# Performance work log

Hardware: AMD Instinct MI355X
Metric: run time of the kernel (lower is better)

## Reference

```python
import jax, jax.numpy as jnp
import numpy as np


def soft_threshold24(w):
    """2:4 soft-threshold along the last dim: in each contiguous group of 4,
    zero the two smallest magnitudes and shrink the two largest by the
    second-smallest magnitude (sign(w) * relu(|w| - t))."""
    M, N = w.shape
    g = w.reshape(M, N // 4, 4)
    a = jnp.abs(g)
    thr = jnp.sort(a, axis=-1)[..., 1:2]  # 2nd-smallest magnitude per group
    s = jnp.sign(g) * jnp.maximum(a - thr, 0.0)
    return s.reshape(M, N)


def mm_fp16(a, b):
    """fake_fp8_mm: cast operands to fp16, accumulate in fp32."""
    return jnp.matmul(a.astype(jnp.float16), b.astype(jnp.float16),
                      preferred_element_type=jnp.float32)


def setup_inputs() -> dict:
    key = jax.random.key(0)
    k0, k1, k2, k3 = jax.random.split(key, 4)
    B, S, D, R = 4, 2048, 2048, 512
    return {
        "x": jax.random.normal(k0, (B, S, D), jnp.float32),
        "weight_in": jax.random.normal(k1, (D, R), jnp.float32) * 0.02,
        "weight_out": jax.random.normal(k2, (D, R), jnp.float32) * 0.02,
        "bias": jax.random.normal(k3, (D,), jnp.float32) * 0.01,
        "sparse_scale_in": jnp.array(1.0, jnp.float32),
        "sparse_scale_out": jnp.array(1.0, jnp.float32),
    }


def reference(x, weight_in, weight_out, bias, sparse_scale_in, sparse_scale_out):
    B, S, D = x.shape
    # stage 1: x @ sparse24(weight_in) * scale_in  -> [B,S,R]
    win_s = soft_threshold24(weight_in) * sparse_scale_in          # [D, R]
    h = mm_fp16(x.reshape(-1, D), win_s)                            # [B*S, R] fp32
    # stage 2: h @ sparse24(weight_out.T) * scale_out + bias -> [B,S,D]
    wout_s = soft_threshold24(weight_out.T) * sparse_scale_out      # [R, D]
    out = mm_fp16(h, wout_s) + bias                                 # [B*S, D]
    return out.reshape(B, S, D)
```

## Files before the change

kernel.cpp:

```cpp
#include <hip/hip_runtime.h>

typedef _Float16 f16;
typedef _Float16 f16x8 __attribute__((ext_vector_type(8)));
typedef float f32x4 __attribute__((ext_vector_type(4)));

__device__ __forceinline__ void g2l16(const void* g, void* l) {
    __builtin_amdgcn_global_load_lds(
        (const __attribute__((address_space(1))) void*)g,
        (__attribute__((address_space(3))) void*)l, 16, 0, 0);
}

template <int N> __device__ __forceinline__ void wait_vmcnt();
template <> __device__ __forceinline__ void wait_vmcnt<0>() { asm volatile("s_waitcnt vmcnt(0)" ::: "memory"); }
template <> __device__ __forceinline__ void wait_vmcnt<4>() { asm volatile("s_waitcnt vmcnt(4)" ::: "memory"); }
template <> __device__ __forceinline__ void wait_vmcnt<6>() { asm volatile("s_waitcnt vmcnt(6)" ::: "memory"); }

__device__ __forceinline__ float soft1(float a, float thr, float w, float s) {
    return copysignf(fmaxf(a - thr, 0.0f), w) * s;
}

__device__ __forceinline__ float thr4(float a0, float a1, float a2, float a3) {
    float lo01 = fminf(a0, a1), hi01 = fmaxf(a0, a1);
    float lo23 = fminf(a2, a3), hi23 = fmaxf(a2, a3);
    return fminf(fmaxf(lo01, lo23), fminf(hi01, hi23));
}

__global__ __launch_bounds__(256) void prep_kernel(
    const float* __restrict__ x, f16* __restrict__ xh, int n8,
    const float* __restrict__ Wi, f16* __restrict__ winT, const float* __restrict__ sci,
    const float* __restrict__ Wo, f16* __restrict__ woutT, const float* __restrict__ sco,
    int D, int R, int nCastB, int nSpInB)
{
    int b = blockIdx.x;
    int tid = threadIdx.x;
    if (b < nCastB) {
        int i = b * 256 + tid;
        if (i < n8) {
            float4 a = reinterpret_cast<const float4*>(x)[2 * i];
            float4 c = reinterpret_cast<const float4*>(x)[2 * i + 1];
            f16x8 o = {(f16)a.x, (f16)a.y, (f16)a.z, (f16)a.w,
                       (f16)c.x, (f16)c.y, (f16)c.z, (f16)c.w};
            reinterpret_cast<f16x8*>(xh)[i] = o;
        }
    } else if (b < nCastB + nSpInB) {
        int t = (b - nCastB) * 256 + tid;
        int RG = R >> 2;
        if (t >= RG * D) return;
        int rg = t / D, d = t - rg * D;
        float s = *sci;
        float4 w = *reinterpret_cast<const float4*>(Wi + (size_t)d * R + rg * 4);
        float a0 = fabsf(w.x), a1 = fabsf(w.y), a2 = fabsf(w.z), a3 = fabsf(w.w);
        float thr = thr4(a0, a1, a2, a3);
        size_t base = (size_t)(rg * 4) * D + d;
        winT[base]                 = (f16)soft1(a0, thr, w.x, s);
        winT[base + D]             = (f16)soft1(a1, thr, w.y, s);
        winT[base + 2 * (size_t)D] = (f16)soft1(a2, thr, w.z, s);
        winT[base + 3 * (size_t)D] = (f16)soft1(a3, thr, w.w, s);
    } else {
        int t = (b - nCastB - nSpInB) * 256 + tid;
        if (t >= (D >> 2) * R) return;
        int dg = t / R, r = t - dg * R;
        float s = *sco;
        size_t i0 = (size_t)(dg * 4) * R + r;
        float w0 = Wo[i0], w1 = Wo[i0 + R], w2 = Wo[i0 + 2 * (size_t)R], w3 = Wo[i0 + 3 * (size_t)R];
        float a0 = fabsf(w0), a1 = fabsf(w1), a2 = fabsf(w2), a3 = fabsf(w3);
        float thr = thr4(a0, a1, a2, a3);
        woutT[i0]                 = (f16)soft1(a0, thr, w0, s);
        woutT[i0 + R]             = (f16)soft1(a1, thr, w1, s);
        woutT[i0 + 2 * (size_t)R] = (f16)soft1(a2, thr, w2, s);
        woutT[i0 + 3 * (size_t)R] = (f16)soft1(a3, thr, w3, s);
    }
}

template <int TBM, int TBN, int TBK, typename OT, bool BIAS>
__global__ __launch_bounds__(256) void gemm_bt(
    const f16* __restrict__ A, const f16* __restrict__ Bt, OT* __restrict__ C,
    const float* __restrict__ bias, int M, int N, int K)
{
    constexpr int KS = TBK / 32;
    constexpr int MI = TBM / 32;
    constexpr int NF = TBN / 32;
    constexpr int HM = TBM / 2;
    constexpr int HN = TBN / 2;
    constexpr int RPO = 512 / TBK;
    constexpr int L  = (TBM + TBN) / 64 * KS;
    __shared__ f16 As[2][TBM * TBK];
    __shared__ f16 Bs[2][TBN * TBK];

    const int tid  = threadIdx.x;
    const int lane = tid & 63;
    const int w    = tid >> 6;
    const int wm   = w & 1;
    const int wn   = w >> 1;
    const int l16  = lane & 15;
    const int quad = lane >> 4;

    const int nbx = N / TBN;
    const int nb  = gridDim.x;
    int d = blockIdx.x;
    int wgid = ((nb & 7) == 0) ? ((d & 7) * (nb >> 3) + (d >> 3)) : d;
    int by = wgid / nbx;
    int bx = wgid - by * nbx;
    const int bm = by * TBM;
    const int bn = bx * TBN;

    constexpr int CPR = TBK / 8;
    const int srow = lane / CPR;
    const int scol = (((lane % CPR) ^ (srow % CPR)) ) * 8;
    const f16* gA = A  + (size_t)(bm + w * (TBM / 4) + srow) * K + scol;
    const f16* gB = Bt + (size_t)(bn + w * (TBN / 4) + srow) * K + scol;

    f32x4 acc[MI][NF] = {};

    auto STAGE = [&](int buf, int t) {
        const size_t k0 = (size_t)t * TBK;
        f16* lA = &As[buf][(w * (TBM / 4)) * TBK];
        f16* lB = &Bs[buf][(w * (TBN / 4)) * TBK];
#pragma unroll
        for (int i = 0; i < (TBM / 4) / RPO; ++i)
            g2l16(gA + k0 + i * RPO * (size_t)K, lA + i * RPO * TBK);
#pragma unroll
        for (int i = 0; i < (TBN / 4) / RPO; ++i)
            g2l16(gB + k0 + i * RPO * (size_t)K, lB + i * RPO * TBK);
    };

    auto LOADFRAG = [&](int buf, f16x8* af, f16x8* bf) {
#pragma unroll
        for (int ks = 0; ks < KS; ++ks) {
            const int xc = (l16 % CPR);
#pragma unroll
            for (int m = 0; m < MI; ++m) {
                int row = wm * HM + m * 16 + l16;
                int ch  = ((ks * 4 + quad) ^ xc) * 8;
                af[m * KS + ks] = *reinterpret_cast<const f16x8*>(&As[buf][row * TBK + ch]);
            }
#pragma unroll
            for (int n = 0; n < NF; ++n) {
                int row = wn * HN + n * 16 + l16;
                int ch  = ((ks * 4 + quad) ^ xc) * 8;
                bf[n * KS + ks] = *reinterpret_cast<const f16x8*>(&Bs[buf][row * TBK + ch]);
            }
        }
    };

    auto MFMA_ALL = [&](f16x8* af, f16x8* bf) {
#pragma unroll
        for (int ks = 0; ks < KS; ++ks)
#pragma unroll
            for (int m = 0; m < MI; ++m)
#pragma unroll
                for (int n = 0; n < NF; ++n)
                    acc[m][n] = __builtin_amdgcn_mfma_f32_16x16x32_f16(
                        af[m * KS + ks], bf[n * KS + ks], acc[m][n], 0, 0, 0);
    };

    const int nk = K / TBK;
    STAGE(0, 0);
    STAGE(1, 1);
    for (int t = 0; t < nk - 2; ++t) {
        wait_vmcnt<L>();
        __builtin_amdgcn_s_barrier();
        __builtin_amdgcn_sched_barrier(0);
        f16x8 af[MI * KS], bf[NF * KS];
        LOADFRAG(t & 1, af, bf);
        asm volatile("s_waitcnt lgkmcnt(0)" ::: "memory");
        __builtin_amdgcn_sched_barrier(0);
        __builtin_amdgcn_s_barrier();
        STAGE(t & 1, t + 2);
        MFMA_ALL(af, bf);
    }
    {
        wait_vmcnt<L>();
        __builtin_amdgcn_s_barrier();
        __builtin_amdgcn_sched_barrier(0);
        f16x8 af[MI * KS], bf[NF * KS];
        LOADFRAG(nk & 1, af, bf);
        MFMA_ALL(af, bf);
    }
    {
        wait_vmcnt<0>();
        __builtin_amdgcn_s_barrier();
        __builtin_amdgcn_sched_barrier(0);
        f16x8 af[MI * KS], bf[NF * KS];
        LOADFRAG((nk - 1) & 1, af, bf);
        MFMA_ALL(af, bf);
    }

#pragma unroll
    for (int m = 0; m < MI; ++m) {
        int row_base = bm + wm * HM + m * 16 + quad * 4;
#pragma unroll
        for (int n = 0; n < NF; ++n) {
            int col = bn + wn * HN + n * 16 + l16;
            float b = BIAS ? bias[col] : 0.0f;
#pragma unroll
            for (int r = 0; r < 4; ++r) {
                float v = acc[m][n][r];
                size_t idx = (size_t)(row_base + r) * N + col;
                if constexpr (BIAS) C[idx] = (OT)(v + b);
                else                C[idx] = (OT)v;
            }
        }
    }
}

extern "C" void kernel_launch(void* const* d_in, const int* in_sizes, int n_in,
                              void* d_out, int out_size, void* d_ws, size_t ws_size,
                              hipStream_t stream)
{
    const float* x      = (const float*)d_in[0];
    const float* w_in   = (const float*)d_in[1];
    const float* w_out  = (const float*)d_in[2];
    const float* bias   = (const float*)d_in[3];
    const float* sc_in  = (const float*)d_in[4];
    const float* sc_out = (const float*)d_in[5];

    const int D = in_sizes[3];
    const int R = in_sizes[1] / D;
    const int M = in_sizes[0] / D;

    f16* winT  = (f16*)d_ws;
    f16* woutT = winT + (size_t)R * D;
    f16* h     = woutT + (size_t)D * R;
    f16* xh    = h + (size_t)M * R;
    float* out = (float*)d_out;

    const int n8 = M * D / 8;
    const int nCastB  = (n8 + 255) / 256;
    const int nSpInB  = ((R / 4) * D + 255) / 256;
    const int nSpOutB = ((D / 4) * R + 255) / 256;
    prep_kernel<<<nCastB + nSpInB + nSpOutB, 256, 0, stream>>>(
        x, xh, n8, w_in, winT, sc_in, w_out, woutT, sc_out, D, R, nCastB, nSpInB);

    gemm_bt<64, 128, 64, f16, false><<<(R / 128) * (M / 64), 256, 0, stream>>>(
        xh, winT, h, nullptr, M, R, D);
    gemm_bt<128, 128, 32, float, true><<<(D / 128) * (M / 128), 256, 0, stream>>>(
        h, woutT, out, bias, M, D, R);
}
```

Baseline: 174.4 us.

## Switch GEMM main loop to triple-buffered LDS with one barrier per step

The GEMM K-loop moves from two LDS buffers to three. Each iteration now issues the next global-to-LDS prefetch into the buffer freed in the previous step, right after a single barrier, so the second barrier per iteration goes away and loads run further ahead of the MFMAs. The prologue and epilogue are rewritten around rotating buffer indices. In exchange, LDS use per block grows by half, which may reduce how many blocks fit on a CU.

```diff
diff --git a/kernel.cpp b/kernel.cpp
--- a/kernel.cpp
+++ b/kernel.cpp
@@ -11,9 +11,9 @@
 }
 
 template <int N> __device__ __forceinline__ void wait_vmcnt();
-template <> __device__ __forceinline__ void wait_vmcnt<0>() { asm volatile("s_waitcnt vmcnt(0)" ::: "memory"); }
-template <> __device__ __forceinline__ void wait_vmcnt<4>() { asm volatile("s_waitcnt vmcnt(4)" ::: "memory"); }
-template <> __device__ __forceinline__ void wait_vmcnt<6>() { asm volatile("s_waitcnt vmcnt(6)" ::: "memory"); }
+template <> __device__ __forceinline__ void wait_vmcnt<0>()  { asm volatile("s_waitcnt vmcnt(0)"  ::: "memory"); }
+template <> __device__ __forceinline__ void wait_vmcnt<4>()  { asm volatile("s_waitcnt vmcnt(4)"  ::: "memory"); }
+template <> __device__ __forceinline__ void wait_vmcnt<6>()  { asm volatile("s_waitcnt vmcnt(6)"  ::: "memory"); }
 
 __device__ __forceinline__ float soft1(float a, float thr, float w, float s) {
     return copysignf(fmaxf(a - thr, 0.0f), w) * s;
@@ -77,6 +77,7 @@
     const f16* __restrict__ A, const f16* __restrict__ Bt, OT* __restrict__ C,
     const float* __restrict__ bias, int M, int N, int K)
 {
+    constexpr int DEPTH = 3;
     constexpr int KS = TBK / 32;
     constexpr int MI = TBM / 32;
     constexpr int NF = TBN / 32;
@@ -84,8 +85,8 @@
     constexpr int HN = TBN / 2;
     constexpr int RPO = 512 / TBK;
     constexpr int L  = (TBM + TBN) / 64 * KS;
-    __shared__ f16 As[2][TBM * TBK];
-    __shared__ f16 Bs[2][TBN * TBK];
+    __shared__ f16 As[DEPTH][TBM * TBK];
+    __shared__ f16 Bs[DEPTH][TBN * TBK];
 
     const int tid  = threadIdx.x;
     const int lane = tid & 63;
@@ -106,7 +107,7 @@
 
     constexpr int CPR = TBK / 8;
     const int srow = lane / CPR;
-    const int scol = (((lane % CPR) ^ (srow % CPR)) ) * 8;
+    const int scol = ((lane % CPR) ^ (srow % CPR)) * 8;
     const f16* gA = A  + (size_t)(bm + w * (TBM / 4) + srow) * K + scol;
     const f16* gB = Bt + (size_t)(bn + w * (TBN / 4) + srow) * K + scol;
 
@@ -125,9 +126,9 @@
     };
 
     auto LOADFRAG = [&](int buf, f16x8* af, f16x8* bf) {
+        const int xc = (l16 % CPR);
 #pragma unroll
         for (int ks = 0; ks < KS; ++ks) {
-            const int xc = (l16 % CPR);
 #pragma unroll
             for (int m = 0; m < MI; ++m) {
                 int row = wm * HM + m * 16 + l16;
@@ -155,34 +156,54 @@
     };
 
     const int nk = K / TBK;
-    STAGE(0, 0);
-    STAGE(1, 1);
-    for (int t = 0; t < nk - 2; ++t) {
-        wait_vmcnt<L>();
-        __builtin_amdgcn_s_barrier();
-        __builtin_amdgcn_sched_barrier(0);
-        f16x8 af[MI * KS], bf[NF * KS];
-        LOADFRAG(t & 1, af, bf);
-        asm volatile("s_waitcnt lgkmcnt(0)" ::: "memory");
-        __builtin_amdgcn_sched_barrier(0);
-        __builtin_amdgcn_s_barrier();
-        STAGE(t & 1, t + 2);
-        MFMA_ALL(af, bf);
-    }
+#pragma unroll
+    for (int p = 0; p < DEPTH; ++p)
+        STAGE(p, p);
+
+    int buf = 0, pbuf = DEPTH - 1;
     {
         wait_vmcnt<L>();
         __builtin_amdgcn_s_barrier();
         __builtin_amdgcn_sched_barrier(0);
         f16x8 af[MI * KS], bf[NF * KS];
-        LOADFRAG(nk & 1, af, bf);
-        MFMA_ALL(af, bf);
+        LOADFRAG(0, af, bf);
+        asm volatile("s_waitcnt lgkmcnt(0)" ::: "memory");
+        __builtin_amdgcn_sched_barrier(0);
+        MFMA_ALL(af, bf);
+        pbuf = 0; buf = 1;
+    }
+    for (int t = 1; t <= nk - DEPTH; ++t) {
+        wait_vmcnt<L>();
+        __builtin_amdgcn_s_barrier();
+        __builtin_amdgcn_sched_barrier(0);
+        STAGE(pbuf, t + DEPTH - 1);
+        __builtin_amdgcn_sched_barrier(0);
+        f16x8 af[MI * KS], bf[NF * KS];
+        LOADFRAG(buf, af, bf);
+        asm volatile("s_waitcnt lgkmcnt(0)" ::: "memory");
+        __builtin_amdgcn_sched_barrier(0);
+        MFMA_ALL(af, bf);
+        pbuf = buf; buf = (buf + 1 == DEPTH) ? 0 : buf + 1;
+    }
+    {
+        wait_vmcnt<L>();
+        __builtin_amdgcn_s_barrier();
+        __builtin_amdgcn_sched_barrier(0);
+        f16x8 af[MI * KS], bf[NF * KS];
+        LOADFRAG(buf, af, bf);
+        asm volatile("s_waitcnt lgkmcnt(0)" ::: "memory");
+        __builtin_amdgcn_sched_barrier(0);
+        MFMA_ALL(af, bf);
+        buf = (buf + 1 == DEPTH) ? 0 : buf + 1;
     }
     {
         wait_vmcnt<0>();
         __builtin_amdgcn_s_barrier();
         __builtin_amdgcn_sched_barrier(0);
         f16x8 af[MI * KS], bf[NF * KS];
-        LOADFRAG((nk - 1) & 1, af, bf);
+        LOADFRAG(buf, af, bf);
+        asm volatile("s_waitcnt lgkmcnt(0)" ::: "memory");
+        __builtin_amdgcn_sched_barrier(0);
         MFMA_ALL(af, bf);
     }
 
```

Measured after the change: 179.2 us. +2.8%, slower.
